# Optimization experiments

Measured on AMD Instinct MI355X. Metric: run time of the kernel, lower is better.

## Reference

```python
import jax, jax.numpy as jnp
import numpy as np

B, T, NEMBD, HEAD = 8, 2048, 1024, 64

def setup_inputs() -> dict:
    key = jax.random.key(0)
    ks = jax.random.split(key, 6)
    return {
        "values": jax.random.normal(ks[0], (B, T, NEMBD), dtype=jnp.float32),
        "keys": jax.random.normal(ks[1], (B, T, NEMBD), dtype=jnp.float32),
        "queries": jax.random.normal(ks[2], (B, T, NEMBD), dtype=jnp.float32),
        "Wk": jax.random.normal(ks[3], (NEMBD, HEAD), dtype=jnp.float32) * (NEMBD ** -0.5),
        "Wq": jax.random.normal(ks[4], (NEMBD, HEAD), dtype=jnp.float32) * (NEMBD ** -0.5),
        "Wv": jax.random.normal(ks[5], (NEMBD, HEAD), dtype=jnp.float32) * (NEMBD ** -0.5),
    }

def reference(values, keys, queries, Wk, Wq, Wv):
    Bq, Tq, C = queries.shape  # C = nEmbd; original scales by C**-0.5 (NOT headSize)
    k = keys @ Wk              # [B,T,H]
    q = queries @ Wq           # [B,T,H]
    v = values @ Wv            # [B,T,H]
    weight = jnp.einsum('bth,bsh->bts', q, k) * (C ** -0.5)  # [B,T,T]
    causal = jnp.tril(jnp.ones((Tq, Tq), dtype=bool))
    weight = jnp.where(causal, weight, -jnp.inf)
    weight = jax.nn.softmax(weight, axis=-1)
    # dropout = 0.0 (eval): identity
    out = jnp.einsum('bts,bsh->bth', weight, v)  # [B,T,H]
    return out
```

## Files before the change

### kernel.cpp

```cpp
#include <hip/hip_runtime.h>
#include <hip/hip_bf16.h>

typedef __bf16 bf16x8 __attribute__((ext_vector_type(8)));
typedef float f32x4 __attribute__((ext_vector_type(4)));
typedef unsigned short u16x8 __attribute__((ext_vector_type(8)));

#define NB 8
#define NT 2048
#define NC 1024
#define NH 64

__device__ __forceinline__ unsigned short bfbits(float f) {
    return __builtin_bit_cast(unsigned short, (__bf16)f);
}

__global__ __launch_bounds__(256) void wt_kernel(const float* __restrict__ Wq,
                                                 const float* __restrict__ Wk,
                                                 const float* __restrict__ Wv,
                                                 unsigned short* __restrict__ Wt) {
    int idx = blockIdx.x * 256 + threadIdx.x;
    int n = idx >> 16;
    int r = idx & 65535;
    int c = r >> 6;
    int h = r & 63;
    const float* W = (n == 0) ? Wq : ((n == 1) ? Wk : Wv);
    float x = W[c * 64 + h];
    Wt[(n << 16) + h * 1024 + c] = bfbits(x);
}

__global__ __launch_bounds__(256, 4) void proj_kernel(const float* __restrict__ Xv,
                                                      const float* __restrict__ Xk,
                                                      const float* __restrict__ Xq,
                                                      const unsigned short* __restrict__ Wt,
                                                      unsigned short* __restrict__ Q,
                                                      unsigned short* __restrict__ K,
                                                      unsigned short* __restrict__ VT) {
    __shared__ __align__(16) char Xs[64 * 256];
    __shared__ __align__(16) char Ws[64 * 256];

    int type = blockIdx.x >> 8;
    int mt   = blockIdx.x & 255;
    int row0 = mt << 6;
    const float* X = (type == 0) ? Xq : ((type == 1) ? Xk : Xv);
    const unsigned short* W = Wt + (type << 16);

    int tid  = threadIdx.x;
    int w    = tid >> 6;
    int lane = tid & 63;
    int lo = lane & 15, hi = lane >> 4;

    f32x4 acc[4];
#pragma unroll
    for (int ct = 0; ct < 4; ++ct) acc[ct] = 0.f;

    for (int kc = 0; kc < 8; ++kc) {
        f32x4 xr[8];
#pragma unroll
        for (int i = 0; i < 8; ++i) {
            int f4 = tid + 256 * i;
            int r  = f4 >> 5, c4 = f4 & 31;
            xr[i] = __builtin_nontemporal_load(
                (const f32x4*)(X + (size_t)(row0 + r) * NC + kc * 128 + c4 * 4));
        }
        u16x8 wr_[4];
#pragma unroll
        for (int i = 0; i < 4; ++i) {
            int s16 = tid + 256 * i;
            int h = s16 >> 4, sl = s16 & 15;
            wr_[i] = *(const u16x8*)(W + h * 1024 + kc * 128 + sl * 8);
        }
        __syncthreads();
#pragma unroll
        for (int i = 0; i < 8; ++i) {
            int f4 = tid + 256 * i;
            int r  = f4 >> 5, c4 = f4 & 31;
            ushort4 bv;
            bv.x = bfbits(xr[i][0]); bv.y = bfbits(xr[i][1]);
            bv.z = bfbits(xr[i][2]); bv.w = bfbits(xr[i][3]);
            int byte = r * 256 + ((c4 * 8) ^ ((r & 7) << 4));
            *(ushort4*)(Xs + byte) = bv;
        }
#pragma unroll
        for (int i = 0; i < 4; ++i) {
            int s16 = tid + 256 * i;
            int h = s16 >> 4, sl = s16 & 15;
            int byte = h * 256 + ((sl * 16) ^ ((h & 7) << 4));
            *(u16x8*)(Ws + byte) = wr_[i];
        }
        __syncthreads();
#pragma unroll
        for (int ks = 0; ks < 4; ++ks) {
            int coff = (ks * 64 + hi * 16) ^ ((lo & 7) << 4);
            bf16x8 af = *(const bf16x8*)(Xs + (w * 16 + lo) * 256 + coff);
#pragma unroll
            for (int ct = 0; ct < 4; ++ct) {
                bf16x8 bf = *(const bf16x8*)(Ws + (ct * 16 + lo) * 256 + coff);
                acc[ct] = __builtin_amdgcn_mfma_f32_16x16x32_bf16(af, bf, acc[ct], 0, 0, 0);
            }
        }
    }

    if (type < 2) {
        unsigned short* O = (type == 0) ? Q : K;
#pragma unroll
        for (int ct = 0; ct < 4; ++ct)
#pragma unroll
            for (int r = 0; r < 4; ++r) {
                int row = row0 + w * 16 + hi * 4 + r;
                int h = lo + 16 * ct;
                O[(size_t)row * NH + h] = bfbits(acc[ct][r]);
            }
    } else {
        int trow = row0 + w * 16 + hi * 4;
        int b = trow >> 11;
        int t = trow & 2047;
#pragma unroll
        for (int ct = 0; ct < 4; ++ct) {
            int h = lo + 16 * ct;
            ushort4 pk;
            pk.x = bfbits(acc[ct][0]);
            pk.y = bfbits(acc[ct][1]);
            pk.z = bfbits(acc[ct][2]);
            pk.w = bfbits(acc[ct][3]);
            *(ushort4*)(VT + (size_t)(b * NH + h) * NT + t) = pk;
        }
    }
}

__global__ __launch_bounds__(256) void attn_kernel(const unsigned short* __restrict__ Q,
                                                   const unsigned short* __restrict__ K,
                                                   const unsigned short* __restrict__ VT,
                                                   float* __restrict__ out) {
    __shared__ __align__(16) unsigned short p_lds[4 * 512];
    __shared__ __align__(16) float acc_lds[4 * 16 * 64];
    __shared__ float l_lds[4][16];

    int b  = blockIdx.x & 7;
    int qt = 127 - (blockIdx.x >> 3);
    int q0 = qt << 4;
    int w    = threadIdx.x >> 6;
    int lane = threadIdx.x & 63;
    int lo = lane & 15, hi = lane >> 4;

    const float SC = 0.03125f * 1.44269504088896340736f;
    const unsigned short* qb = Q + (size_t)(b * NT + q0 + lo) * NH + hi * 8;
    bf16x8 qr0 = *(const bf16x8*)(qb);
    bf16x8 qr1 = *(const bf16x8*)(qb + 32);
    bf16x8 qf0, qf1;
#pragma unroll
    for (int jj = 0; jj < 8; ++jj) {
        qf0[jj] = (__bf16)((float)qr0[jj] * SC);
        qf1[jj] = (__bf16)((float)qr1[jj] * SC);
    }

    int Ctot = (q0 + 47) >> 5;
    int c0 = (Ctot * w) >> 2;
    int c1 = (Ctot * (w + 1)) >> 2;

    float l[4];
    f32x4 acc[4];
#pragma unroll
    for (int r = 0; r < 4; ++r) l[r] = 0.f;
#pragma unroll
    for (int ct = 0; ct < 4; ++ct) acc[ct] = 0.f;

    unsigned short* pl = p_lds + w * 512;

    const unsigned short* kp = K + (size_t)(b * NT + (c0 << 5) + lo) * NH + hi * 8;
    bf16x8 kn0 = *(const bf16x8*)(kp);
    bf16x8 kn1 = *(const bf16x8*)(kp + 32);
    bf16x8 kn2 = *(const bf16x8*)(kp + 16 * NH);
    bf16x8 kn3 = *(const bf16x8*)(kp + 16 * NH + 32);

    for (int c = c0; c < c1; ++c) {
        int s0 = c << 5;
        bf16x8 k0 = kn0, k1 = kn1, k2 = kn2, k3 = kn3;
        if (c + 1 < c1) {
            const unsigned short* kp2 = K + (size_t)(b * NT + ((c + 1) << 5) + lo) * NH + hi * 8;
            kn0 = *(const bf16x8*)(kp2);
            kn1 = *(const bf16x8*)(kp2 + 32);
            kn2 = *(const bf16x8*)(kp2 + 16 * NH);
            kn3 = *(const bf16x8*)(kp2 + 16 * NH + 32);
        }
        f32x4 S0 = 0.f, S1 = 0.f;
        S0 = __builtin_amdgcn_mfma_f32_16x16x32_bf16(qf0, k0, S0, 0, 0, 0);
        S0 = __builtin_amdgcn_mfma_f32_16x16x32_bf16(qf1, k1, S0, 0, 0, 0);
        S1 = __builtin_amdgcn_mfma_f32_16x16x32_bf16(qf0, k2, S1, 0, 0, 0);
        S1 = __builtin_amdgcn_mfma_f32_16x16x32_bf16(qf1, k3, S1, 0, 0, 0);

        const unsigned short* vb = VT + (size_t)(b * NH + lo) * NT + s0 + hi * 8;
        bf16x8 vv0 = *(const bf16x8*)(vb);
        bf16x8 vv1 = *(const bf16x8*)(vb + 16 * NT);
        bf16x8 vv2 = *(const bf16x8*)(vb + 32 * NT);
        bf16x8 vv3 = *(const bf16x8*)(vb + 48 * NT);

        int s_a = s0 + lo, s_b = s0 + 16 + lo;
        float p0[4], p1[4];
#pragma unroll
        for (int r = 0; r < 4; ++r) {
            int qi = q0 + hi * 4 + r;
            p0[r] = (s_a <= qi) ? exp2f(S0[r] - 32.f) : 0.f;
            p1[r] = (s_b <= qi) ? exp2f(S1[r] - 32.f) : 0.f;
            l[r] += p0[r] + p1[r];
            int ql = hi * 4 + r;
            pl[ql * 32 + lo]      = bfbits(p0[r]);
            pl[ql * 32 + 16 + lo] = bfbits(p1[r]);
        }
        bf16x8 pa = *(const bf16x8*)(pl + lo * 32 + hi * 8);
        acc[0] = __builtin_amdgcn_mfma_f32_16x16x32_bf16(pa, vv0, acc[0], 0, 0, 0);
        acc[1] = __builtin_amdgcn_mfma_f32_16x16x32_bf16(pa, vv1, acc[1], 0, 0, 0);
        acc[2] = __builtin_amdgcn_mfma_f32_16x16x32_bf16(pa, vv2, acc[2], 0, 0, 0);
        acc[3] = __builtin_amdgcn_mfma_f32_16x16x32_bf16(pa, vv3, acc[3], 0, 0, 0);
    }

#pragma unroll
    for (int d = 1; d < 16; d <<= 1)
#pragma unroll
        for (int r = 0; r < 4; ++r)
            l[r] += __shfl_xor(l[r], d, 16);

#pragma unroll
    for (int r = 0; r < 4; ++r) {
        int ql = hi * 4 + r;
#pragma unroll
        for (int ct = 0; ct < 4; ++ct)
            acc_lds[(w * 16 + ql) * 64 + lo + 16 * ct] = acc[ct][r];
    }
    if (lo == 0) {
#pragma unroll
        for (int r = 0; r < 4; ++r)
            l_lds[w][hi * 4 + r] = l[r];
    }
    __syncthreads();

    int q  = threadIdx.x >> 4;
    int h0 = (threadIdx.x & 15) << 2;
    float L = l_lds[0][q] + l_lds[1][q] + l_lds[2][q] + l_lds[3][q];
    float ox = 0.f, oy = 0.f, oz = 0.f, ow = 0.f;
#pragma unroll
    for (int ww = 0; ww < 4; ++ww) {
        const float* p = acc_lds + (ww * 16 + q) * 64 + h0;
        ox += p[0]; oy += p[1]; oz += p[2]; ow += p[3];
    }
    float inv = 1.0f / L;
    float4 res = make_float4(ox * inv, oy * inv, oz * inv, ow * inv);
    *(float4*)(out + (size_t)(b * NT + q0 + q) * NH + h0) = res;
}

extern "C" void kernel_launch(void* const* d_in, const int* in_sizes, int n_in,
                              void* d_out, int out_size, void* d_ws, size_t ws_size,
                              hipStream_t stream) {
    const float* values  = (const float*)d_in[0];
    const float* keys    = (const float*)d_in[1];
    const float* queries = (const float*)d_in[2];
    const float* Wk = (const float*)d_in[3];
    const float* Wq = (const float*)d_in[4];
    const float* Wv = (const float*)d_in[5];
    float* out = (float*)d_out;

    unsigned short* Wt = (unsigned short*)d_ws;
    unsigned short* Qb = Wt + 196608;
    unsigned short* Kb = Qb + 1048576;
    unsigned short* VT = Kb + 1048576;

    wt_kernel<<<768, 256, 0, stream>>>(Wq, Wk, Wv, Wt);
    proj_kernel<<<768, 256, 0, stream>>>(values, keys, queries, Wt, Qb, Kb, VT);
    attn_kernel<<<1024, 256, 0, stream>>>(Qb, Kb, VT, out);
}
```

Measured before the change: 84.77 us.

## Widen attention key chunks to 64 and swizzle P tile in LDS

The per-wave inner loop now covers 64 keys per iteration instead of 32. It issues eight QK MFMAs and eight PV MFMAs per step, and the V loads move ahead of the K prefetch so they are in flight earlier. The probability tile in shared memory doubles in size and uses an XOR swizzle on its byte offsets to avoid LDS bank conflicts when rows are read back as 8-wide vectors. The aim is to amortize loop overhead and memory latency over more work. The cost is more register pressure and coarser splitting of keys across the four waves, which may leave them less evenly loaded on short query tiles.

Result: no change. 83.94 us (-1.0%).

```diff
diff --git a/kernel.cpp b/kernel.cpp
--- a/kernel.cpp
+++ b/kernel.cpp
@@ -131,7 +131,7 @@
                                                    const unsigned short* __restrict__ K,
                                                    const unsigned short* __restrict__ VT,
                                                    float* __restrict__ out) {
-    __shared__ __align__(16) unsigned short p_lds[4 * 512];
+    __shared__ __align__(16) unsigned short p_lds[4 * 1024];
     __shared__ __align__(16) float acc_lds[4 * 16 * 64];
     __shared__ float l_lds[4][16];
 
@@ -153,9 +153,9 @@
         qf1[jj] = (__bf16)((float)qr1[jj] * SC);
     }
 
-    int Ctot = (q0 + 47) >> 5;
-    int c0 = (Ctot * w) >> 2;
-    int c1 = (Ctot * (w + 1)) >> 2;
+    int Ct = (q0 + 79) >> 6;
+    int c0 = (Ct * w) >> 2;
+    int c1 = (Ct * (w + 1)) >> 2;
 
     float l[4];
     f32x4 acc[4];
@@ -164,53 +164,79 @@
 #pragma unroll
     for (int ct = 0; ct < 4; ++ct) acc[ct] = 0.f;
 
-    unsigned short* pl = p_lds + w * 512;
-
-    const unsigned short* kp = K + (size_t)(b * NT + (c0 << 5) + lo) * NH + hi * 8;
-    bf16x8 kn0 = *(const bf16x8*)(kp);
-    bf16x8 kn1 = *(const bf16x8*)(kp + 32);
-    bf16x8 kn2 = *(const bf16x8*)(kp + 16 * NH);
-    bf16x8 kn3 = *(const bf16x8*)(kp + 16 * NH + 32);
+    unsigned short* pl = p_lds + w * 1024;
+    char* plb = (char*)pl;
+
+    bf16x8 kn[8];
+    {
+        const unsigned short* kp = K + (size_t)(b * NT + (c0 << 6) + lo) * NH + hi * 8;
+#pragma unroll
+        for (int g = 0; g < 4; ++g) {
+            kn[2 * g]     = *(const bf16x8*)(kp + g * 16 * NH);
+            kn[2 * g + 1] = *(const bf16x8*)(kp + g * 16 * NH + 32);
+        }
+    }
 
     for (int c = c0; c < c1; ++c) {
-        int s0 = c << 5;
-        bf16x8 k0 = kn0, k1 = kn1, k2 = kn2, k3 = kn3;
+        int s0 = c << 6;
+        bf16x8 kk[8];
+#pragma unroll
+        for (int i = 0; i < 8; ++i) kk[i] = kn[i];
+        const unsigned short* vb = VT + (size_t)(b * NH + lo) * NT + s0 + hi * 8;
+        bf16x8 vA0 = *(const bf16x8*)(vb);
+        bf16x8 vA1 = *(const bf16x8*)(vb + 16 * NT);
+        bf16x8 vA2 = *(const bf16x8*)(vb + 32 * NT);
+        bf16x8 vA3 = *(const bf16x8*)(vb + 48 * NT);
+        bf16x8 vB0 = *(const bf16x8*)(vb + 32);
+        bf16x8 vB1 = *(const bf16x8*)(vb + 16 * NT + 32);
+        bf16x8 vB2 = *(const bf16x8*)(vb + 32 * NT + 32);
+        bf16x8 vB3 = *(const bf16x8*)(vb + 48 * NT + 32);
         if (c + 1 < c1) {
-            const unsigned short* kp2 = K + (size_t)(b * NT + ((c + 1) << 5) + lo) * NH + hi * 8;
-            kn0 = *(const bf16x8*)(kp2);
-            kn1 = *(const bf16x8*)(kp2 + 32);
-            kn2 = *(const bf16x8*)(kp2 + 16 * NH);
-            kn3 = *(const bf16x8*)(kp2 + 16 * NH + 32);
-        }
-        f32x4 S0 = 0.f, S1 = 0.f;
-        S0 = __builtin_amdgcn_mfma_f32_16x16x32_bf16(qf0, k0, S0, 0, 0, 0);
-        S0 = __builtin_amdgcn_mfma_f32_16x16x32_bf16(qf1, k1, S0, 0, 0, 0);
-        S1 = __builtin_amdgcn_mfma_f32_16x16x32_bf16(qf0, k2, S1, 0, 0, 0);
-        S1 = __builtin_amdgcn_mfma_f32_16x16x32_bf16(qf1, k3, S1, 0, 0, 0);
-
-        const unsigned short* vb = VT + (size_t)(b * NH + lo) * NT + s0 + hi * 8;
-        bf16x8 vv0 = *(const bf16x8*)(vb);
-        bf16x8 vv1 = *(const bf16x8*)(vb + 16 * NT);
-        bf16x8 vv2 = *(const bf16x8*)(vb + 32 * NT);
-        bf16x8 vv3 = *(const bf16x8*)(vb + 48 * NT);
-
-        int s_a = s0 + lo, s_b = s0 + 16 + lo;
-        float p0[4], p1[4];
+            const unsigned short* kp2 = K + (size_t)(b * NT + ((c + 1) << 6) + lo) * NH + hi * 8;
+#pragma unroll
+            for (int g = 0; g < 4; ++g) {
+                kn[2 * g]     = *(const bf16x8*)(kp2 + g * 16 * NH);
+                kn[2 * g + 1] = *(const bf16x8*)(kp2 + g * 16 * NH + 32);
+            }
+        }
+
+        f32x4 S[4];
+#pragma unroll
+        for (int t = 0; t < 4; ++t) {
+            f32x4 s = 0.f;
+            s = __builtin_amdgcn_mfma_f32_16x16x32_bf16(qf0, kk[2 * t], s, 0, 0, 0);
+            s = __builtin_amdgcn_mfma_f32_16x16x32_bf16(qf1, kk[2 * t + 1], s, 0, 0, 0);
+            S[t] = s;
+        }
+
 #pragma unroll
         for (int r = 0; r < 4; ++r) {
             int qi = q0 + hi * 4 + r;
-            p0[r] = (s_a <= qi) ? exp2f(S0[r] - 32.f) : 0.f;
-            p1[r] = (s_b <= qi) ? exp2f(S1[r] - 32.f) : 0.f;
-            l[r] += p0[r] + p1[r];
             int ql = hi * 4 + r;
-            pl[ql * 32 + lo]      = bfbits(p0[r]);
-            pl[ql * 32 + 16 + lo] = bfbits(p1[r]);
-        }
-        bf16x8 pa = *(const bf16x8*)(pl + lo * 32 + hi * 8);
-        acc[0] = __builtin_amdgcn_mfma_f32_16x16x32_bf16(pa, vv0, acc[0], 0, 0, 0);
-        acc[1] = __builtin_amdgcn_mfma_f32_16x16x32_bf16(pa, vv1, acc[1], 0, 0, 0);
-        acc[2] = __builtin_amdgcn_mfma_f32_16x16x32_bf16(pa, vv2, acc[2], 0, 0, 0);
-        acc[3] = __builtin_amdgcn_mfma_f32_16x16x32_bf16(pa, vv3, acc[3], 0, 0, 0);
+            int sw = (ql & 7) << 4;
+            float psum = 0.f;
+#pragma unroll
+            for (int t = 0; t < 4; ++t) {
+                int sk = s0 + t * 16 + lo;
+                float p = (sk <= qi) ? exp2f(S[t][r] - 32.f) : 0.f;
+                psum += p;
+                int byte = ql * 128 + ((((t * 16 + lo) * 2)) ^ sw);
+                *(unsigned short*)(plb + byte) = bfbits(p);
+            }
+            l[r] += psum;
+        }
+
+        int rsw = (lo & 7) << 4;
+        bf16x8 pa0 = *(const bf16x8*)(plb + lo * 128 + ((hi * 16) ^ rsw));
+        bf16x8 pa1 = *(const bf16x8*)(plb + lo * 128 + (((4 + hi) * 16) ^ rsw));
+        acc[0] = __builtin_amdgcn_mfma_f32_16x16x32_bf16(pa0, vA0, acc[0], 0, 0, 0);
+        acc[1] = __builtin_amdgcn_mfma_f32_16x16x32_bf16(pa0, vA1, acc[1], 0, 0, 0);
+        acc[2] = __builtin_amdgcn_mfma_f32_16x16x32_bf16(pa0, vA2, acc[2], 0, 0, 0);
+        acc[3] = __builtin_amdgcn_mfma_f32_16x16x32_bf16(pa0, vA3, acc[3], 0, 0, 0);
+        acc[0] = __builtin_amdgcn_mfma_f32_16x16x32_bf16(pa1, vB0, acc[0], 0, 0, 0);
+        acc[1] = __builtin_amdgcn_mfma_f32_16x16x32_bf16(pa1, vB1, acc[1], 0, 0, 0);
+        acc[2] = __builtin_amdgcn_mfma_f32_16x16x32_bf16(pa1, vB2, acc[2], 0, 0, 0);
+        acc[3] = __builtin_amdgcn_mfma_f32_16x16x32_bf16(pa1, vB3, acc[3], 0, 0, 0);
     }
 
 #pragma unroll
```
